# Performance work log

Hardware: AMD Instinct MI355X
Metric: run time of the kernel (lower is better)

Reference implementation:

```python
import jax, jax.numpy as jnp
import numpy as np

T = 0.07  # temperature from __init__ default


def setup_inputs() -> dict:
    key = jax.random.key(0)
    ks = jax.random.split(key, 5)
    B, D, H, E = 4096, 2048, 2048, 128
    init = lambda k, shp, fan: jax.random.normal(k, shp, dtype=jnp.float32) * (1.0 / np.sqrt(fan))
    return {
        "input1": jax.random.normal(ks[0], (B, D), dtype=jnp.float32),
        "input2": jax.random.normal(ks[1], (B, D), dtype=jnp.float32),
        "W0": init(ks[2], (D, H), D), "b0": jnp.zeros((H,), jnp.float32),
        "W1": init(ks[3], (H, H), H), "b1": jnp.zeros((H,), jnp.float32),
        "W2": init(ks[4], (H, E), H), "b2": jnp.zeros((E,), jnp.float32),
    }


def _mlp(x, W0, b0, W1, b1, W2, b2):
    # Linear -> ReLU -> Linear -> Linear (ReLU only between hidden layers)
    x = jax.nn.relu(x @ W0 + b0)
    x = x @ W1 + b1
    return x @ W2 + b2


def reference(input1, input2, W0, b0, W1, b1, W2, b2):
    B = input1.shape[0]
    e1 = _mlp(input1, W0, b0, W1, b1, W2, b2)
    e2 = _mlp(input2, W0, b0, W1, b1, W2, b2)
    feats = jnp.stack([e1, e2], axis=1)                       # [B, 2, E]
    feats = feats / jnp.linalg.norm(feats, axis=2, keepdims=True)
    # view(N,2,dim).permute(1,0,2).reshape(2N,dim): view0 rows then view1 rows
    f = jnp.concatenate([feats[:, 0], feats[:, 1]], axis=0)   # [2B, E]
    N2 = 2 * B
    sim = (f @ f.T) / T                                        # [2B, 2B]
    idx = jnp.arange(N2)
    pos = sim[idx, (idx + B) % N2]                             # partner view similarity
    # exclude self-similarity (diagonal) from the logsumexp denominator
    sim = jnp.where(jnp.eye(N2, dtype=bool), jnp.float32(-1e9), sim)
    # CE with positive at index 0 of [pos, negatives] == -pos + logsumexp(non-self)
    loss = jnp.mean(jax.nn.logsumexp(sim, axis=1) - pos)
    return loss
```

## Files before the change

### kernel.cpp

```cpp
#include <hip/hip_runtime.h>
#include <stdint.h>

typedef float f32x4 __attribute__((ext_vector_type(4)));
typedef float f32x16 __attribute__((ext_vector_type(16)));
typedef __bf16 bf16x8 __attribute__((ext_vector_type(8)));
typedef unsigned short u16;
typedef unsigned int u32;

#define INVT 14.285714285714286f
#define L2E  1.4426950408889634f

__device__ __forceinline__ u16 f2bf(float f) {
  u32 u = __float_as_uint(f);
  u32 r = (u + 0x7fffu + ((u >> 16) & 1u)) >> 16;
  return (u16)r;
}
__device__ __forceinline__ float bf2f(u16 h) { return __uint_as_float(((u32)h) << 16); }

__device__ __forceinline__ void g2l16(const void* g, void* l) {
  auto gp = reinterpret_cast<__attribute__((address_space(1))) uint32_t*>(
      reinterpret_cast<uintptr_t>(g));
  auto lp = reinterpret_cast<__attribute__((address_space(3))) uint32_t*>(
      reinterpret_cast<uintptr_t>(l));
  __builtin_amdgcn_global_load_lds(gp, lp, 16, 0, 0);
}


__global__ __launch_bounds__(256) void k_prep(const float* __restrict__ in1,
                                              const float* __restrict__ in2,
                                              u16* __restrict__ Xb,
                                              const float* __restrict__ w0, u16* __restrict__ w0t,
                                              const float* __restrict__ w1, u16* __restrict__ w1t,
                                              const float* __restrict__ w2, u16* __restrict__ w2t) {
  const int bid = blockIdx.x;
  const int tid = threadIdx.x;
  if (bid < 8192) {
    const int l = tid & 63, w = tid >> 6;
    const int lm = l & 31, ch = l >> 5;
    const int u = bid * 4 + w;
    const int s = u & 127, g = u >> 7;
    const float* src = (g < 128 ? in1 : in2) +
                       (size_t)((g & 127) * 32 + lm) * 2048 + s * 16 + ch * 8;
    float4 v0 = *(const float4*)src;
    float4 v1 = *(const float4*)(src + 4);
    uint4 o;
    o.x = (u32)f2bf(v0.x) | ((u32)f2bf(v0.y) << 16);
    o.y = (u32)f2bf(v0.z) | ((u32)f2bf(v0.w) << 16);
    o.z = (u32)f2bf(v1.x) | ((u32)f2bf(v1.y) << 16);
    o.w = (u32)f2bf(v1.z) | ((u32)f2bf(v1.w) << 16);
    *(uint4*)(Xb + (size_t)s * 131072 + g * 512 + l * 8) = o;
    return;
  }
  if (bid < 12288) {
    const int l = tid & 63, w = tid >> 6;
    const int lm = l & 31, ch = l >> 5;
    const int v = (bid - 8192) * 4 + w;
    const int z = v >> 13, u2 = v & 8191;
    const int s = u2 & 127, g = u2 >> 7;
    const float* Wm = z ? w1 : w0;
    u16* O = z ? w1t : w0t;
    const float* src = Wm + (size_t)(s * 16 + ch * 8) * 2048 + g * 32 + lm;
    float f0 = src[0];
    float f1 = src[2048];
    float f2 = src[2 * 2048];
    float f3 = src[3 * 2048];
    float f4 = src[4 * 2048];
    float f5 = src[5 * 2048];
    float f6 = src[6 * 2048];
    float f7 = src[7 * 2048];
    uint4 o;
    o.x = (u32)f2bf(f0) | ((u32)f2bf(f1) << 16);
    o.y = (u32)f2bf(f2) | ((u32)f2bf(f3) << 16);
    o.z = (u32)f2bf(f4) | ((u32)f2bf(f5) << 16);
    o.w = (u32)f2bf(f6) | ((u32)f2bf(f7) << 16);
    *(uint4*)(O + (size_t)s * 32768 + g * 512 + l * 8) = o;
    return;
  }
  __shared__ float t[64][65];
  const int f = bid - 12288;
  const float* in = w2;
  u16* out = w2t;
  const int C = 128, R = 2048;
  const int r0 = (f >> 1) * 64, c0t = (f & 1) * 64;
#pragma unroll
  for (int p = 0; p < 16; ++p) {
    int idx = p * 256 + tid;
    int r = idx >> 6, c = idx & 63;
    t[r][c] = in[(size_t)(r0 + r) * C + (c0t + c)];
  }
  __syncthreads();
#pragma unroll
  for (int p = 0; p < 16; ++p) {
    int idx = p * 256 + tid;
    int c = idx >> 6, r = idx & 63;
    out[(size_t)(c0t + c) * R + (r0 + r)] = f2bf(t[r][c]);
  }
}

__global__ __launch_bounds__(512, 2) void k_gemm(const u16* __restrict__ A, const u16* __restrict__ Bt,
                                                 const float* __restrict__ bias, u16* __restrict__ C,
                                                 int M, int N, int K, int relu, int blockedC) {
  __shared__ __align__(16) u16 sm[65536];
  const int tid = threadIdx.x;
  const int l = tid & 63, w = tid >> 6;
  const int wm = w >> 2, wn = w & 3;
  const int lm = l & 31, c0 = l >> 5;
  const int m0 = blockIdx.y * 256, n0 = blockIdx.x * 256;

  const char* gA = (const char*)A + (size_t)((m0 >> 5) + w) * 1024 + l * 16;
  const char* gB = (const char*)Bt + (size_t)((n0 >> 5) + w) * 1024 + l * 16;
  const size_t slabA = (size_t)M * 32, slabB = (size_t)N * 32;

  auto issue_half = [&](int t, int part, int stg) {
    const int h = part >> 1, isB = part & 1;
    const char* g = isB ? gB : gA;
    const size_t slab = isB ? slabB : slabA;
    const int s0 = t * 4 + h * 2;
    char* lb = (char*)sm + stg * 65536 + isB * 32768 + h * 16384 + w * 1024 + l * 16;
    g2l16(g + (size_t)s0 * slab, lb);
    g2l16(g + (size_t)(s0 + 1) * slab, lb + 8192);
  };

  f32x16 acc[4][2] = {};
  const int NT = K >> 6;

  issue_half(0, 0, 0); issue_half(0, 1, 0); issue_half(0, 2, 0); issue_half(0, 3, 0);
  asm volatile("s_waitcnt vmcnt(4)" ::: "memory");
  asm volatile("s_barrier" ::: "memory");

  for (int kt = 0; kt < NT; ++kt) {
    const u16* bcur = sm + (kt & 1) * 32768;
    const int nstg = (kt & 1) ^ 1;
    const bool pf = (kt + 1) < NT;

#pragma unroll
    for (int k = 0; k < 4; ++k) {
      const u16* As = bcur + (k >> 1) * 8192;
      const u16* Bs = bcur + 16384 + (k >> 1) * 8192;
      const int fb = (k & 1) * 4096 + c0 * 256 + lm * 8;
      bf16x8 a4[4], b2[2];
#pragma unroll
      for (int fm = 0; fm < 4; ++fm)
        a4[fm] = *(const bf16x8*)(As + fb + (wm * 4 + fm) * 512);
#pragma unroll
      for (int fn = 0; fn < 2; ++fn)
        b2[fn] = *(const bf16x8*)(Bs + fb + (wn * 2 + fn) * 512);
      if (pf) issue_half(kt + 1, k, nstg);
      asm volatile("s_barrier" ::: "memory");
      asm volatile("s_waitcnt lgkmcnt(0)" ::: "memory");
      __builtin_amdgcn_s_setprio(1);
#pragma unroll
      for (int fm = 0; fm < 4; ++fm)
#pragma unroll
        for (int fn = 0; fn < 2; ++fn)
          acc[fm][fn] = __builtin_amdgcn_mfma_f32_32x32x16_bf16(a4[fm], b2[fn],
                                                                acc[fm][fn], 0, 0, 0);
      __builtin_amdgcn_s_setprio(0);
      if (k & 1) {
        if (pf) asm volatile("s_waitcnt vmcnt(4)" ::: "memory");
        else    asm volatile("s_waitcnt vmcnt(0)" ::: "memory");
      }
      asm volatile("s_barrier" ::: "memory");
    }
  }

  if (blockedC) {
#pragma unroll
    for (int fn = 0; fn < 2; ++fn) {
      const int col = n0 + wn * 64 + lm + fn * 32;
      const float b = bias[col];
      const int sc = col >> 4, cb = (col >> 3) & 1, e = col & 7;
#pragma unroll
      for (int fm = 0; fm < 4; ++fm) {
        const int gg = (m0 >> 5) + wm * 4 + fm;
        u16* base = C + (size_t)sc * ((size_t)M * 16) + gg * 512 + cb * 256 + e;
#pragma unroll
        for (int g = 0; g < 4; ++g)
#pragma unroll
          for (int rr = 0; rr < 4; ++rr) {
            float v = acc[fm][fn][g * 4 + rr] + b;
            if (relu) v = fmaxf(v, 0.0f);
            base[(4 * c0 + g * 8 + rr) * 8] = f2bf(v);
          }
      }
    }
  } else {
    const int colb = n0 + wn * 64 + lm;
    const int rowb = m0 + wm * 128 + 4 * c0;
#pragma unroll
    for (int fn = 0; fn < 2; ++fn) {
      const float b = bias[colb + fn * 32];
#pragma unroll
      for (int fm = 0; fm < 4; ++fm)
#pragma unroll
        for (int g = 0; g < 4; ++g)
#pragma unroll
          for (int rr = 0; rr < 4; ++rr) {
            float v = acc[fm][fn][g * 4 + rr] + b;
            if (relu) v = fmaxf(v, 0.0f);
            C[(size_t)(rowb + fm * 32 + g * 8 + rr) * N + colb + fn * 32] = f2bf(v);
          }
    }
  }
}

__global__ __launch_bounds__(256, 2) void k_gemm_sk(const u16* __restrict__ A, const u16* __restrict__ Bt,
                                                    float* __restrict__ Ep, int K, int Ksplit) {
  __shared__ __align__(16) u16 sm[24576];
  const int tid = threadIdx.x;
  const int l = tid & 63, w = tid >> 6;
  const int wm = w >> 1, wn = w & 1;
  const int m0 = blockIdx.y * 128;
  const int split = blockIdx.x;
  const int k0s = split * Ksplit;

  const int kb = ((l & 3) ^ ((l >> 3) & 3)) * 16;
  const char* gA = (const char*)(A + (size_t)(m0 + w * 16 + (l >> 2)) * K + k0s) + kb;
  const char* gB = (const char*)(Bt + (size_t)(w * 16 + (l >> 2)) * K + k0s) + kb;
  const size_t radv = (size_t)64 * K * 2;

  auto issue = [&](int kcB, int stg) {
    char* base = (char*)sm + stg * 16384;
    char* dA = base + w * 1024 + l * 16;
    char* dB = base + 8192 + w * 1024 + l * 16;
    g2l16(gA + kcB, dA);
    g2l16(gA + radv + kcB, dA + 4096);
    g2l16(gB + kcB, dB);
    g2l16(gB + radv + kcB, dB + 4096);
  };

  const int lm = l & 31;
  const int c0 = l >> 5;
  const int sw = (lm >> 1) & 3;

  f32x16 acc[2][2] = {};

  auto compute = [&](int stg) {
    const u16* As = sm + stg * 8192;
    const u16* Bs = As + 4096;
#pragma unroll
    for (int t = 0; t < 2; ++t) {
      const int cc = (((t << 1) + c0) ^ sw) * 8;
      bf16x8 a2[2], b2[2];
#pragma unroll
      for (int fm = 0; fm < 2; ++fm) a2[fm] = *(const bf16x8*)(As + (wm * 64 + fm * 32 + lm) * 32 + cc);
#pragma unroll
      for (int fn = 0; fn < 2; ++fn) b2[fn] = *(const bf16x8*)(Bs + (wn * 64 + fn * 32 + lm) * 32 + cc);
#pragma unroll
      for (int fm = 0; fm < 2; ++fm)
#pragma unroll
        for (int fn = 0; fn < 2; ++fn)
          acc[fm][fn] = __builtin_amdgcn_mfma_f32_32x32x16_bf16(a2[fm], b2[fn],
                                                                acc[fm][fn], 0, 0, 0);
    }
  };

  const int NK = Ksplit >> 5;
  issue(0, 0);
  issue(64, 1);
  int st = 0;
  for (int kt = 0; kt < NK; ++kt) {
    if (kt + 1 < NK) asm volatile("s_waitcnt vmcnt(4)" ::: "memory");
    else             asm volatile("s_waitcnt vmcnt(0)" ::: "memory");
    asm volatile("s_barrier" ::: "memory");
    if (kt + 2 < NK) {
      int stp = st + 2; if (stp >= 3) stp -= 3;
      issue((kt + 2) * 64, stp);
    }
    compute(st);
    ++st; if (st == 3) st = 0;
  }

  const int colb = wn * 64 + lm;
  const int rowb = m0 + wm * 64 + 4 * c0;
#pragma unroll
  for (int fn = 0; fn < 2; ++fn)
#pragma unroll
    for (int fm = 0; fm < 2; ++fm)
#pragma unroll
      for (int g = 0; g < 4; ++g)
#pragma unroll
        for (int rr = 0; rr < 4; ++rr)
          Ep[((size_t)split * 8192 + rowb + fm * 32 + g * 8 + rr) * 128 + colb + fn * 32] =
              acc[fm][fn][g * 4 + rr];
}

__global__ __launch_bounds__(256) void k_norm(const float* __restrict__ Ep,
                                              const float* __restrict__ b2, u16* __restrict__ F) {
  const int l = threadIdx.x & 63, w = threadIdx.x >> 6;
  const int row = blockIdx.x * 4 + w;
  const float2* base = (const float2*)Ep + (size_t)row * 64 + l;
  float x = 0.f, y = 0.f;
#pragma unroll
  for (int s = 0; s < 4; ++s) {
    float2 t = base[(size_t)s * (8192 * 64)];
    x += t.x; y += t.y;
  }
  x += b2[l * 2]; y += b2[l * 2 + 1];
  float sq = x * x + y * y;
#pragma unroll
  for (int off = 1; off < 64; off <<= 1) sq += __shfl_xor(sq, off);
  const float inv = 1.0f / sqrtf(sq);
  F[(size_t)row * 128 + l * 2] = f2bf(x * inv);
  F[(size_t)row * 128 + l * 2 + 1] = f2bf(y * inv);
}

__global__ __launch_bounds__(256, 2) void k_sim(const u16* __restrict__ F, float* __restrict__ Sp) {
  __shared__ __align__(16) u16 sm[32768];
  const int tid = threadIdx.x;
  const int l = tid & 63, w = tid >> 6;
  const int wm = w >> 1, wn = w & 1;
  const int lm = l & 31, c0 = l >> 5;
  const int r0 = blockIdx.y * 128;
  const int cb0 = blockIdx.x * 1024;

  u16* B0 = sm;
  u16* AB1 = sm + 16384;

  const int srow0 = tid >> 4;
  const int schunk = tid & 15;
  auto stage = [&](const u16* src, u16* dst) {
#pragma unroll
    for (int j = 0; j < 8; ++j) {
      const int row = j * 16 + srow0;
      const int lc = schunk ^ (row & 7);
      g2l16((const char*)(src + (size_t)row * 128) + lc * 16,
            (char*)dst + j * 4096 + tid * 16);
    }
  };

  stage(F + (size_t)r0 * 128, AB1);
  asm volatile("s_waitcnt vmcnt(0)" ::: "memory");
  __syncthreads();

  bf16x8 a[2][8];
#pragma unroll
  for (int fm = 0; fm < 2; ++fm) {
    const int ra = wm * 64 + fm * 32 + lm;
#pragma unroll
    for (int kf = 0; kf < 8; ++kf)
      a[fm][kf] = *(const bf16x8*)(AB1 + ra * 128 + (((kf << 1) + c0) ^ (ra & 7)) * 8);
  }
  asm volatile("s_waitcnt lgkmcnt(0)" ::: "memory");

  stage(F + (size_t)cb0 * 128, B0);

  const float S2 = INVT * L2E;
  const int rB = wn * 64 + lm;
  f32x16 runS[2] = {};

#pragma unroll 1
  for (int p = 0; p < 8; ++p) {
    asm volatile("s_waitcnt vmcnt(0)" ::: "memory");
    asm volatile("s_barrier" ::: "memory");
    if (p < 7) stage(F + (size_t)(cb0 + (p + 1) * 128) * 128, (p & 1) ? B0 : AB1);
    const u16* Bs = (p & 1) ? AB1 : B0;

    f32x16 acc[2][2] = {};
#pragma unroll
    for (int kf = 0; kf < 8; ++kf) {
      const int kc = (kf << 1) + c0;
      bf16x8 b0v = *(const bf16x8*)(Bs + rB * 128 + (kc ^ (rB & 7)) * 8);
      bf16x8 b1v = *(const bf16x8*)(Bs + (rB + 32) * 128 + (kc ^ ((rB + 32) & 7)) * 8);
      acc[0][0] = __builtin_amdgcn_mfma_f32_32x32x16_bf16(a[0][kf], b0v, acc[0][0], 0, 0, 0);
      acc[0][1] = __builtin_amdgcn_mfma_f32_32x32x16_bf16(a[0][kf], b1v, acc[0][1], 0, 0, 0);
      acc[1][0] = __builtin_amdgcn_mfma_f32_32x32x16_bf16(a[1][kf], b0v, acc[1][0], 0, 0, 0);
      acc[1][1] = __builtin_amdgcn_mfma_f32_32x32x16_bf16(a[1][kf], b1v, acc[1][1], 0, 0, 0);
    }

    const int cp = cb0 + p * 128;
    if (cp == r0) {
#pragma unroll
      for (int fm = 0; fm < 2; ++fm)
#pragma unroll
        for (int fn = 0; fn < 2; ++fn) {
          const int rcol = wn * 64 + fn * 32 + lm;
#pragma unroll
          for (int r = 0; r < 16; ++r) {
            const int rrow = wm * 64 + fm * 32 + (r & 3) + 8 * (r >> 2) + 4 * c0;
            float e = exp2f(fmaf(acc[fm][fn][r], S2, -S2));
            if (rrow == rcol) e = 0.f;
            runS[fm][r] += e;
          }
        }
    } else {
#pragma unroll
      for (int fm = 0; fm < 2; ++fm)
#pragma unroll
        for (int fn = 0; fn < 2; ++fn)
#pragma unroll
          for (int r = 0; r < 16; ++r)
            runS[fm][r] += exp2f(fmaf(acc[fm][fn][r], S2, -S2));
    }
  }

#pragma unroll
  for (int fm = 0; fm < 2; ++fm)
#pragma unroll
    for (int r = 0; r < 16; ++r) {
      float s = runS[fm][r];
      s += __shfl_xor(s, 1);
      s += __shfl_xor(s, 2);
      s += __shfl_xor(s, 4);
      s += __shfl_xor(s, 8);
      s += __shfl_xor(s, 16);
      runS[fm][r] = s;
    }

  __syncthreads();
  float* red = (float*)sm;
  if (wn == 0) {
    if (lm == 0) {
#pragma unroll
      for (int fm = 0; fm < 2; ++fm)
#pragma unroll
        for (int r = 0; r < 16; ++r)
          red[wm * 64 + fm * 32 + (r & 3) + 8 * (r >> 2) + 4 * c0] = runS[fm][r];
    }
  }
  __syncthreads();
  if (wn == 1 && lm == 0) {
#pragma unroll
    for (int fm = 0; fm < 2; ++fm)
#pragma unroll
      for (int r = 0; r < 16; ++r) {
        const int rr = wm * 64 + fm * 32 + (r & 3) + 8 * (r >> 2) + 4 * c0;
        Sp[(size_t)blockIdx.x * 8192 + r0 + rr] = red[rr] + runS[fm][r];
      }
  }
}

__global__ __launch_bounds__(256) void k_combine(const float* __restrict__ Sp,
                                                 const u16* __restrict__ F,
                                                 float* __restrict__ out) {
  const int r = blockIdx.x * 256 + threadIdx.x;
  float S = 0.f;
#pragma unroll
  for (int c = 0; c < 8; ++c) S += Sp[c * 8192 + r];
  const float lse = INVT + logf(S);
  const int par = (r + 4096) & 8191;
  const bf16x8* a = (const bf16x8*)(F + (size_t)r * 128);
  const bf16x8* b = (const bf16x8*)(F + (size_t)par * 128);
  float dot = 0.f;
#pragma unroll
  for (int k = 0; k < 16; ++k) {
    bf16x8 va = a[k], vb = b[k];
#pragma unroll
    for (int j = 0; j < 8; ++j) dot = fmaf((float)va[j], (float)vb[j], dot);
  }
  float contrib = lse - dot * INVT;
#pragma unroll
  for (int off = 1; off < 64; off <<= 1) contrib += __shfl_xor(contrib, off);
  if ((threadIdx.x & 63) == 0) atomicAdd(out, contrib * (1.0f / 8192.0f));
}

extern "C" void kernel_launch(void* const* d_in, const int* in_sizes, int n_in,
                              void* d_out, int out_size, void* d_ws, size_t ws_size,
                              hipStream_t stream) {
  const float* input1 = (const float*)d_in[0];
  const float* input2 = (const float*)d_in[1];
  const float* W0 = (const float*)d_in[2];
  const float* b0 = (const float*)d_in[3];
  const float* W1 = (const float*)d_in[4];
  const float* b1 = (const float*)d_in[5];
  const float* W2 = (const float*)d_in[6];
  const float* b2 = (const float*)d_in[7];
  float* out = (float*)d_out;
  char* ws = (char*)d_ws;

  u16* Xb = (u16*)(ws + 0);
  u16* H1 = (u16*)(ws + 33554432);
  u16* W0T = (u16*)(ws + 67108864);
  u16* W1T = (u16*)(ws + 75497472);
  float* Ep = (float*)(ws + 67108864);
  u16* W2T = (u16*)(ws + 83886080);
  float* Sp = (float*)(ws + 83886080);
  u16* Ff = (u16*)(ws + 84410368);
  u16* H2 = Xb;

  hipMemsetAsync(d_out, 0, sizeof(float), stream);
  k_prep<<<12352, 256, 0, stream>>>(input1, input2, Xb, W0, W0T, W1, W1T, W2, W2T);
  k_gemm<<<dim3(8, 32), 512, 0, stream>>>(Xb, W0T, b0, H1, 8192, 2048, 2048, 1, 1);
  k_gemm<<<dim3(8, 32), 512, 0, stream>>>(H1, W1T, b1, H2, 8192, 2048, 2048, 0, 0);
  k_gemm_sk<<<dim3(4, 64), 256, 0, stream>>>(H2, W2T, Ep, 2048, 512);
  k_norm<<<2048, 256, 0, stream>>>(Ep, b2, Ff);
  k_sim<<<dim3(8, 64), 256, 0, stream>>>(Ff, Sp);
  k_combine<<<32, 256, 0, stream>>>(Sp, Ff, out);
}
```

Before: 339.6 us.

## Tile input bf16 conversion through LDS, remap GEMM blocks per XCD, add sched barriers

```diff
diff --git a/kernel.cpp b/kernel.cpp
--- a/kernel.cpp
+++ b/kernel.cpp
@@ -34,27 +34,38 @@
                                               const float* __restrict__ w2, u16* __restrict__ w2t) {
   const int bid = blockIdx.x;
   const int tid = threadIdx.x;
-  if (bid < 8192) {
+  if (bid < 2048) {
+    __shared__ u16 tl[64][136];
+    const int rb = bid >> 4, cb = bid & 15;
+    const int R0 = rb * 64, C0 = cb * 128;
+    const float* src = (R0 < 4096 ? in1 : in2);
+    const int Rs = (R0 < 4096 ? R0 : R0 - 4096);
+    const int r = tid >> 2;
+    const int cbase = (tid & 3) * 8;
+#pragma unroll
+    for (int p = 0; p < 4; ++p) {
+      const int c = cbase + p * 32;
+      const float* sp = src + (size_t)(Rs + r) * 2048 + C0 + c;
+      float4 v0 = *(const float4*)sp;
+      float4 v1 = *(const float4*)(sp + 4);
+      u16* d = &tl[r][c];
+      d[0] = f2bf(v0.x); d[1] = f2bf(v0.y); d[2] = f2bf(v0.z); d[3] = f2bf(v0.w);
+      d[4] = f2bf(v1.x); d[5] = f2bf(v1.y); d[6] = f2bf(v1.z); d[7] = f2bf(v1.w);
+    }
+    __syncthreads();
+    const int u = tid >> 4, t16 = tid & 15;
+    const int g = u >> 3, s = u & 7;
+    const int c0 = t16 >> 3, lmb = (t16 & 7) * 4;
+    u16* dst = Xb + (size_t)(cb * 8 + s) * 131072 + (rb * 2 + g) * 512 + t16 * 32;
+#pragma unroll
+    for (int q = 0; q < 4; ++q)
+      *(uint4*)(dst + q * 8) = *(const uint4*)&tl[g * 32 + lmb + q][s * 16 + c0 * 8];
+    return;
+  }
+  if (bid < 6144) {
     const int l = tid & 63, w = tid >> 6;
     const int lm = l & 31, ch = l >> 5;
-    const int u = bid * 4 + w;
-    const int s = u & 127, g = u >> 7;
-    const float* src = (g < 128 ? in1 : in2) +
-                       (size_t)((g & 127) * 32 + lm) * 2048 + s * 16 + ch * 8;
-    float4 v0 = *(const float4*)src;
-    float4 v1 = *(const float4*)(src + 4);
-    uint4 o;
-    o.x = (u32)f2bf(v0.x) | ((u32)f2bf(v0.y) << 16);
-    o.y = (u32)f2bf(v0.z) | ((u32)f2bf(v0.w) << 16);
-    o.z = (u32)f2bf(v1.x) | ((u32)f2bf(v1.y) << 16);
-    o.w = (u32)f2bf(v1.z) | ((u32)f2bf(v1.w) << 16);
-    *(uint4*)(Xb + (size_t)s * 131072 + g * 512 + l * 8) = o;
-    return;
-  }
-  if (bid < 12288) {
-    const int l = tid & 63, w = tid >> 6;
-    const int lm = l & 31, ch = l >> 5;
-    const int v = (bid - 8192) * 4 + w;
+    const int v = (bid - 2048) * 4 + w;
     const int z = v >> 13, u2 = v & 8191;
     const int s = u2 & 127, g = u2 >> 7;
     const float* Wm = z ? w1 : w0;
@@ -77,7 +88,7 @@
     return;
   }
   __shared__ float t[64][65];
-  const int f = bid - 12288;
+  const int f = bid - 6144;
   const float* in = w2;
   u16* out = w2t;
   const int C = 128, R = 2048;
@@ -105,7 +116,12 @@
   const int l = tid & 63, w = tid >> 6;
   const int wm = w >> 2, wn = w & 3;
   const int lm = l & 31, c0 = l >> 5;
-  const int m0 = blockIdx.y * 256, n0 = blockIdx.x * 256;
+
+  const int bid0 = blockIdx.y * 8 + blockIdx.x;
+  const int xcd = bid0 & 7, slot = bid0 >> 3;
+  const int bx = (xcd & 1) * 4 + (slot & 3);
+  const int by = (xcd >> 1) * 8 + (slot >> 2);
+  const int m0 = by * 256, n0 = bx * 256;
 
   const char* gA = (const char*)A + (size_t)((m0 >> 5) + w) * 1024 + l * 16;
   const char* gB = (const char*)Bt + (size_t)((n0 >> 5) + w) * 1024 + l * 16;
@@ -148,6 +164,7 @@
       if (pf) issue_half(kt + 1, k, nstg);
       asm volatile("s_barrier" ::: "memory");
       asm volatile("s_waitcnt lgkmcnt(0)" ::: "memory");
+      __builtin_amdgcn_sched_barrier(0);
       __builtin_amdgcn_s_setprio(1);
 #pragma unroll
       for (int fm = 0; fm < 4; ++fm)
@@ -156,6 +173,7 @@
           acc[fm][fn] = __builtin_amdgcn_mfma_f32_32x32x16_bf16(a4[fm], b2[fn],
                                                                 acc[fm][fn], 0, 0, 0);
       __builtin_amdgcn_s_setprio(0);
+      __builtin_amdgcn_sched_barrier(0);
       if (k & 1) {
         if (pf) asm volatile("s_waitcnt vmcnt(4)" ::: "memory");
         else    asm volatile("s_waitcnt vmcnt(0)" ::: "memory");
@@ -479,7 +497,7 @@
   u16* H2 = Xb;
 
   hipMemsetAsync(d_out, 0, sizeof(float), stream);
-  k_prep<<<12352, 256, 0, stream>>>(input1, input2, Xb, W0, W0T, W1, W1T, W2, W2T);
+  k_prep<<<6208, 256, 0, stream>>>(input1, input2, Xb, W0, W0T, W1, W1T, W2, W2T);
   k_gemm<<<dim3(8, 32), 512, 0, stream>>>(Xb, W0T, b0, H1, 8192, 2048, 2048, 1, 1);
   k_gemm<<<dim3(8, 32), 512, 0, stream>>>(H1, W1T, b1, H2, 8192, 2048, 2048, 0, 0);
   k_gemm_sk<<<dim3(4, 64), 256, 0, stream>>>(H2, W2T, Ep, 2048, 512);
```

Result: faster. 325.6 us (-4.1%).
